# Performance work log

Measured on AMD Instinct MI355X. Metric: run time of the kernel, lower is better.

Reference implementation:

```python
import jax, jax.numpy as jnp
import numpy as np

SAMPLING_RATIO = 1.0


def gcn_conv(x, src, dst, ew, W, b):
    """PyG GCNConv: h = D^-1/2 (A+I) D^-1/2 (xW) + b, edges weighted by ew.
    Masked edges (ew=0) contribute neither messages nor degree, exactly
    matching running the conv on the subset edge_index."""
    n = x.shape[0]
    h = x @ W                                              # [N, out]
    deg = jax.ops.segment_sum(ew, dst, num_segments=n) + 1.0  # +1 for self-loop
    dinv = jax.lax.rsqrt(deg)                              # deg >= 1, safe
    norm = dinv[src] * dinv[dst] * ew                      # [E]
    agg = jax.ops.segment_sum(h[src] * norm[:, None], dst, num_segments=n)
    return agg + h * (dinv * dinv)[:, None] + b            # self-loop term + bias


def setup_inputs() -> dict:
    key = jax.random.key(0)
    ks = jax.random.split(key, 8)
    N, E, F_IN, HID, OUT = 50000, 800000, 128, 128, 64
    x = jax.random.normal(ks[0], (N, F_IN), dtype=jnp.float32)
    edge_index = jax.random.randint(ks[1], (2, E), 0, N, dtype=jnp.int32)
    edge_rand = jax.random.uniform(ks[2], (E,), dtype=jnp.float32)
    s0 = 1.0 / np.sqrt(F_IN)
    s1 = 1.0 / np.sqrt(HID)
    w0 = jax.random.normal(ks[3], (F_IN, HID), dtype=jnp.float32) * s0
    b0 = jnp.zeros((HID,), dtype=jnp.float32)
    w1 = jax.random.normal(ks[4], (HID, HID), dtype=jnp.float32) * s1
    b1 = jnp.zeros((HID,), dtype=jnp.float32)
    w2 = jax.random.normal(ks[5], (HID, OUT), dtype=jnp.float32) * s1
    b2 = jnp.zeros((OUT,), dtype=jnp.float32)
    return {"x": x, "edge_index": edge_index, "edge_rand": edge_rand,
            "w0": w0, "b0": b0, "w1": w1, "b1": b1, "w2": w2, "b2": b2}


def reference(x, edge_index, edge_rand, w0, b0, w1, b1, w2, b2):
    src, dst = edge_index[0], edge_index[1]
    ones = jnp.ones(src.shape, dtype=x.dtype)
    # first pass over full graph -> tmp_z
    z = jax.nn.relu(gcn_conv(x, src, dst, ones, w0, b0))
    z = jax.nn.relu(gcn_conv(z, src, dst, ones, w1, b1))
    tmp_z = gcn_conv(z, src, dst, ones, w2, b2)
    # edge sampling: gather-dot-sigmoid-threshold (detached mask)
    edge_logit = jnp.sum(tmp_z[src] * tmp_z[dst], axis=-1)
    edge_weight = jax.nn.sigmoid(edge_logit)
    mask = jax.lax.stop_gradient(
        (edge_weight > SAMPLING_RATIO * edge_rand).astype(x.dtype))
    # second pass: sampled edges for hidden layers, full edges for last layer
    h = jax.nn.relu(gcn_conv(x, src, dst, mask, w0, b0))
    h = jax.nn.relu(gcn_conv(h, src, dst, mask, w1, b1))
    out = gcn_conv(h, src, dst, ones, w2, b2)
    return out
```

## Files before the change

### kernel.cpp

```cpp
#include <hip/hip_runtime.h>


typedef __attribute__((ext_vector_type(8))) short bf16x8;
typedef __attribute__((ext_vector_type(4))) float f32x4;

__device__ inline unsigned bfpair(float lo, float hi) {
    unsigned a = __float_as_uint(lo), b = __float_as_uint(hi);
    a = (a + 0x7FFFu + ((a >> 16) & 1u)) >> 16;
    b = (b + 0x7FFFu + ((b >> 16) & 1u)) & 0xFFFF0000u;
    return a | b;
}
__device__ inline unsigned short bf1(float v) {
    unsigned u = __float_as_uint(v);
    return (unsigned short)((u + 0x7FFFu + ((u >> 16) & 1u)) >> 16);
}
__device__ inline void unpack2(unsigned u, float& f0, float& f1) {
    f0 = __uint_as_float(u << 16);
    f1 = __uint_as_float(u & 0xFFFF0000u);
}

__global__ void k_scan1(const int* __restrict__ in, int* __restrict__ out,
                        int* __restrict__ bsums, int N) {
    __shared__ int tmp[256];
    int i = blockIdx.x * 256 + threadIdx.x;
    int v = (i < N) ? in[i] : 0;
    tmp[threadIdx.x] = v;
    __syncthreads();
    for (int off = 1; off < 256; off <<= 1) {
        int t = (threadIdx.x >= off) ? tmp[threadIdx.x - off] : 0;
        __syncthreads();
        tmp[threadIdx.x] += t;
        __syncthreads();
    }
    if (i < N) out[i] = tmp[threadIdx.x] - v;
    if (threadIdx.x == 255) bsums[blockIdx.x] = tmp[255];
}

__global__ void k_scan2(int* __restrict__ bsums, int nb) {
    __shared__ int tmp[256];
    int v = (threadIdx.x < nb) ? bsums[threadIdx.x] : 0;
    tmp[threadIdx.x] = v;
    __syncthreads();
    for (int off = 1; off < 256; off <<= 1) {
        int t = (threadIdx.x >= off) ? tmp[threadIdx.x - off] : 0;
        __syncthreads();
        tmp[threadIdx.x] += t;
        __syncthreads();
    }
    if (threadIdx.x < nb) bsums[threadIdx.x] = tmp[threadIdx.x] - v;
}

__global__ void k_scan3(int* __restrict__ out, const int* __restrict__ bsums, int N, int E) {
    int i = blockIdx.x * 256 + threadIdx.x;
    if (i < N) out[i] += bsums[blockIdx.x];
    if (i == 0) out[N] = E;
}

__global__ __launch_bounds__(256) void k_bcount(const int* __restrict__ dst,
                                                int* __restrict__ cnt, int E, int chunk) {
    __shared__ int h[1024];
    for (int i = threadIdx.x; i < 1024; i += 256) h[i] = 0;
    __syncthreads();
    int beg = blockIdx.x * chunk, end = min(E, beg + chunk);
    for (int e = beg + threadIdx.x; e < end; e += 256)
        atomicAdd(&h[dst[e] >> 6], 1);
    __syncthreads();
    for (int b = threadIdx.x; b < 1024; b += 256)
        cnt[b * 64 + blockIdx.x] = h[b];
}

__global__ __launch_bounds__(256) void k_bscatter(const int* __restrict__ src,
                                                  const int* __restrict__ dst,
                                                  const float* __restrict__ er,
                                                  const int* __restrict__ sbase,
                                                  int2* __restrict__ stg, int E, int chunk) {
    __shared__ int cur[1024];
    for (int i = threadIdx.x; i < 1024; i += 256) cur[i] = 0;
    __syncthreads();
    int beg = blockIdx.x * chunk, end = min(E, beg + chunk);
    for (int e = beg + threadIdx.x; e < end; e += 256) {
        int d = dst[e];
        int b = d >> 6;
        int loc = atomicAdd(&cur[b], 1);
        int pos = sbase[b * 64 + blockIdx.x] + loc;
        stg[pos] = make_int2(src[e] | ((d & 63) << 16), (int)__float_as_uint(er[e]));
    }
}

__global__ __launch_bounds__(256) void k_bindeg(const int2* __restrict__ stg,
                                                const int* __restrict__ sbase,
                                                int* __restrict__ indeg,
                                                float* __restrict__ dinvF, int N) {
    __shared__ int cnt[64];
    if (threadIdx.x < 64) cnt[threadIdx.x] = 0;
    __syncthreads();
    int b = blockIdx.x;
    int beg = sbase[b * 64], end = sbase[(b + 1) * 64];
    for (int i = beg + threadIdx.x; i < end; i += 256)
        atomicAdd(&cnt[(stg[i].x >> 16) & 63], 1);
    __syncthreads();
    if (threadIdx.x < 64) {
        int node = b * 64 + threadIdx.x;
        if (node < N) {
            int c = cnt[threadIdx.x];
            indeg[node] = c;
            dinvF[node] = 1.0f / sqrtf((float)c + 1.0f);
        }
    }
}

__global__ __launch_bounds__(256) void k_bfill(const int2* __restrict__ stg,
                                               const int* __restrict__ sbase,
                                               const int* __restrict__ csr_off,
                                               int2* __restrict__ csr_se, int N) {
    __shared__ int cur[64];
    int b = blockIdx.x;
    if (threadIdx.x < 64) {
        int node = b * 64 + threadIdx.x;
        cur[threadIdx.x] = (node < N) ? csr_off[node] : 0;
    }
    __syncthreads();
    int beg = sbase[b * 64], end = sbase[(b + 1) * 64];
    for (int i = beg + threadIdx.x; i < end; i += 256) {
        int2 se = stg[i];
        int j = (se.x >> 16) & 63;
        int pos = atomicAdd(&cur[j], 1);
        csr_se[pos] = make_int2(se.x & 0xFFFF, se.y);
    }
}

__global__ __launch_bounds__(128) void k_surv(const float* __restrict__ tz,
                                              const int* __restrict__ csr_off,
                                              const int2* __restrict__ csr_se,
                                              float* __restrict__ survive,
                                              float* __restrict__ dinvM, int N) {
    const int v = blockIdx.x;
    const int l = threadIdx.x & 15;
    const int s = threadIdx.x >> 4;
    const int e0 = csr_off[v];
    const int e1 = csr_off[v + 1];
    const float4 tv = *(const float4*)&tz[(size_t)v * 64 + l * 4];
    int cnt = 0;
    for (int i = e0 + s; i < e1; i += 8) {
        int2 se = csr_se[i];
        const float4 a = *(const float4*)&tz[(size_t)se.x * 64 + l * 4];
        float p = a.x * tv.x + a.y * tv.y + a.z * tv.z + a.w * tv.w;
        p += __shfl_xor(p, 1, 16);
        p += __shfl_xor(p, 2, 16);
        p += __shfl_xor(p, 4, 16);
        p += __shfl_xor(p, 8, 16);
        float sg = 1.0f / (1.0f + expf(-p));
        float m = (sg > __uint_as_float((unsigned)se.y)) ? 1.0f : 0.0f;
        if (l == 0) {
            survive[i] = m;
            cnt += (m != 0.0f) ? 1 : 0;
        }
    }
    __shared__ int sc[8];
    if (l == 0) sc[s] = cnt;
    __syncthreads();
    if (threadIdx.x == 0) {
        int t = 0;
#pragma unroll
        for (int k = 0; k < 8; k++) t += sc[k];
        dinvM[v] = 1.0f / sqrtf((float)t + 1.0f);
    }
}

__device__ inline void packw3_one(const float* __restrict__ W, unsigned short* __restrict__ Wp,
                                  int OUTC, int idx) {
    int l = idx & 63;
    int tk = idx >> 6;
    int kb = tk & 3;
    int ct = tk >> 2;
    size_t PL = (size_t)(OUTC / 16) * 4 * 64 * 8;
    unsigned short v0[8], v1[8], v2[8];
#pragma unroll
    for (int i = 0; i < 8; i++) {
        float wv = W[(kb * 32 + ((l >> 4) * 8) + i) * OUTC + ct * 16 + (l & 15)];
        unsigned short h0 = bf1(wv);
        float f0 = __uint_as_float((unsigned)h0 << 16);
        float r1 = wv - f0;
        unsigned short h1 = bf1(r1);
        float f1 = __uint_as_float((unsigned)h1 << 16);
        unsigned short h2 = bf1(r1 - f1);
        v0[i] = h0; v1[i] = h1; v2[i] = h2;
    }
    auto st = [](unsigned short* dst, unsigned short* v) {
        uint4 u;
        u.x = v[0] | ((unsigned)v[1] << 16);
        u.y = v[2] | ((unsigned)v[3] << 16);
        u.z = v[4] | ((unsigned)v[5] << 16);
        u.w = v[6] | ((unsigned)v[7] << 16);
        *(uint4*)dst = u;
    };
    st(&Wp[(size_t)idx * 8], v0);
    st(&Wp[PL + (size_t)idx * 8], v1);
    st(&Wp[2 * PL + (size_t)idx * 8], v2);
}

__global__ void k_packw3_all(const float* __restrict__ w0, const float* __restrict__ w1,
                             const float* __restrict__ w2,
                             unsigned short* __restrict__ w0p, unsigned short* __restrict__ w1p,
                             unsigned short* __restrict__ w2p) {
    int b = blockIdx.x;
    if (b < 8) packw3_one(w0, w0p, 128, b * 256 + threadIdx.x);
    else if (b < 16) packw3_one(w1, w1p, 128, (b - 8) * 256 + threadIdx.x);
    else packw3_one(w2, w2p, 64, (b - 16) * 256 + threadIdx.x);
}

template <int OUTC, bool WB16>
__global__ __launch_bounds__(256) void k_gemm_split(const float* __restrict__ A,
                                                    const unsigned short* __restrict__ Wp,
                                                    float* __restrict__ Cout,
                                                    unsigned short* __restrict__ Cb, int N) {
    constexpr int CT = OUTC / 16;
    constexpr int PL = CT * 4 * 64 * 8;
    constexpr int LDW = OUTC + 4;
    __shared__ float eps[64 * LDW];
    const int w = threadIdx.x >> 6;
    const int l = threadIdx.x & 63;
    int row = blockIdx.x * 64 + w * 16 + (l & 15);
    int rowc = (row < N) ? row : (N - 1);

    bf16x8 a0[4], a1[4], a2[4];
#pragma unroll
    for (int kb = 0; kb < 4; kb++) {
        const float* pa = &A[(size_t)rowc * 128 + kb * 32 + ((l >> 4) * 8)];
        float4 x0 = *(const float4*)pa;
        float4 x1 = *(const float4*)(pa + 4);
        float xa[8] = {x0.x, x0.y, x0.z, x0.w, x1.x, x1.y, x1.z, x1.w};
#pragma unroll
        for (int i = 0; i < 8; i++) {
            unsigned short h0 = bf1(xa[i]);
            float f0 = __uint_as_float((unsigned)h0 << 16);
            float r1 = xa[i] - f0;
            unsigned short h1 = bf1(r1);
            float f1 = __uint_as_float((unsigned)h1 << 16);
            unsigned short h2 = bf1(r1 - f1);
            a0[kb][i] = (short)h0;
            a1[kb][i] = (short)h1;
            a2[kb][i] = (short)h2;
        }
    }
#pragma unroll
    for (int ct = 0; ct < CT; ct++) {
        f32x4 accA = {0.f, 0.f, 0.f, 0.f};
        f32x4 accB = {0.f, 0.f, 0.f, 0.f};
#pragma unroll
        for (int kb = 0; kb < 4; kb++) {
            const size_t bo = ((size_t)(ct * 4 + kb) * 64 + l) * 8;
            bf16x8 b0 = *(const bf16x8*)&Wp[bo];
            bf16x8 b1 = *(const bf16x8*)&Wp[PL + bo];
            bf16x8 b2 = *(const bf16x8*)&Wp[2 * PL + bo];
            accA = __builtin_amdgcn_mfma_f32_16x16x32_bf16(a0[kb], b0, accA, 0, 0, 0);
            accB = __builtin_amdgcn_mfma_f32_16x16x32_bf16(a0[kb], b1, accB, 0, 0, 0);
            accA = __builtin_amdgcn_mfma_f32_16x16x32_bf16(a1[kb], b0, accA, 0, 0, 0);
            accB = __builtin_amdgcn_mfma_f32_16x16x32_bf16(a1[kb], b1, accB, 0, 0, 0);
            accA = __builtin_amdgcn_mfma_f32_16x16x32_bf16(a2[kb], b0, accA, 0, 0, 0);
            accB = __builtin_amdgcn_mfma_f32_16x16x32_bf16(a0[kb], b2, accB, 0, 0, 0);
        }
#pragma unroll
        for (int r = 0; r < 4; r++) {
            int rr = w * 16 + (l >> 4) * 4 + r;
            eps[rr * LDW + ct * 16 + (l & 15)] = accA[r] + accB[r];
        }
    }
    __syncthreads();
    constexpr int NF4 = 64 * OUTC / 4;
    for (int idx = threadIdx.x; idx < NF4; idx += 256) {
        int rl = idx / (OUTC / 4);
        int cg = idx % (OUTC / 4);
        int grow = blockIdx.x * 64 + rl;
        if (grow < N) {
            const float* sp = &eps[rl * LDW + cg * 4];
            float4 vv = make_float4(sp[0], sp[1], sp[2], sp[3]);
            *(float4*)&Cout[(size_t)grow * OUTC + cg * 4] = vv;
            if (WB16)
                *(uint2*)&Cb[(size_t)grow * OUTC + cg * 4] =
                    make_uint2(bfpair(vv.x, vv.y), bfpair(vv.z, vv.w));
        }
    }
}

template <int OUTC>
__global__ __launch_bounds__(256) void k_gemm_mfma(const unsigned short* __restrict__ A,
                                                   const unsigned short* __restrict__ Wpk,
                                                   unsigned short* __restrict__ C, int N) {
    constexpr int CT = OUTC / 16;
    __shared__ unsigned short eps[64 * OUTC];
    const int w = threadIdx.x >> 6;
    const int l = threadIdx.x & 63;
    const int rowl = (w * 16) + (l & 15);
    int row = blockIdx.x * 64 + rowl;
    int rowc = (row < N) ? row : (N - 1);

    bf16x8 a[4];
#pragma unroll
    for (int kb = 0; kb < 4; kb++)
        a[kb] = *(const bf16x8*)&A[(size_t)rowc * 128 + kb * 32 + ((l >> 4) * 8)];

#pragma unroll
    for (int ct = 0; ct < CT; ct++) {
        f32x4 acc = {0.f, 0.f, 0.f, 0.f};
#pragma unroll
        for (int kb = 0; kb < 4; kb++) {
            bf16x8 b = *(const bf16x8*)&Wpk[((size_t)(ct * 4 + kb) * 64 + l) * 8];
            acc = __builtin_amdgcn_mfma_f32_16x16x32_bf16(a[kb], b, acc, 0, 0, 0);
        }
#pragma unroll
        for (int r = 0; r < 4; r++) {
            int rr = w * 16 + (l >> 4) * 4 + r;
            eps[rr * OUTC + ct * 16 + (l & 15)] = bf1(acc[r]);
        }
    }
    __syncthreads();
    constexpr int NU4 = 64 * OUTC / 8;
    for (int idx = threadIdx.x; idx < NU4; idx += 256) {
        int rl = idx / (OUTC / 8);
        int cg = idx % (OUTC / 8);
        int grow = blockIdx.x * 64 + rl;
        if (grow < N)
            *(uint4*)&C[(size_t)grow * OUTC + cg * 8] = *(const uint4*)&eps[rl * OUTC + cg * 8];
    }
}

template <bool RELU>
__global__ __launch_bounds__(128) void k_agg128(const float* __restrict__ h,
                                                const int* __restrict__ csr_off,
                                                const int2* __restrict__ csr_se,
                                                const float* __restrict__ dinv,
                                                const float* __restrict__ bias,
                                                float* __restrict__ out, int N) {
    const int v = blockIdx.x;
    const int l = threadIdx.x & 31;
    const int s = threadIdx.x >> 5;
    const int e0 = csr_off[v];
    const int e1 = csr_off[v + 1];
    float4 acc = make_float4(0.f, 0.f, 0.f, 0.f);
    int i = e0 + s;
    for (; i + 4 < e1; i += 8) {
        int sa = csr_se[i].x;      float wa = dinv[sa];
        int sb = csr_se[i + 4].x;  float wb = dinv[sb];
        float4 a = *(const float4*)&h[(size_t)sa * 128 + l * 4];
        float4 b = *(const float4*)&h[(size_t)sb * 128 + l * 4];
        acc.x = fmaf(a.x, wa, acc.x); acc.y = fmaf(a.y, wa, acc.y);
        acc.z = fmaf(a.z, wa, acc.z); acc.w = fmaf(a.w, wa, acc.w);
        acc.x = fmaf(b.x, wb, acc.x); acc.y = fmaf(b.y, wb, acc.y);
        acc.z = fmaf(b.z, wb, acc.z); acc.w = fmaf(b.w, wb, acc.w);
    }
    if (i < e1) {
        int sa = csr_se[i].x;
        float wa = dinv[sa];
        float4 a = *(const float4*)&h[(size_t)sa * 128 + l * 4];
        acc.x = fmaf(a.x, wa, acc.x); acc.y = fmaf(a.y, wa, acc.y);
        acc.z = fmaf(a.z, wa, acc.z); acc.w = fmaf(a.w, wa, acc.w);
    }
    __shared__ float4 red[4][32];
    red[s][l] = acc;
    __syncthreads();
    if (threadIdx.x < 32) {
        float4 r0 = red[0][l], r1 = red[1][l], r2 = red[2][l], r3 = red[3][l];
        float dv = dinv[v];
        float4 hv = *(const float4*)&h[(size_t)v * 128 + l * 4];
        float4 bb = *(const float4*)&bias[l * 4];
        float4 o;
        o.x = dv * ((r0.x + r1.x + r2.x + r3.x) + hv.x * dv) + bb.x;
        o.y = dv * ((r0.y + r1.y + r2.y + r3.y) + hv.y * dv) + bb.y;
        o.z = dv * ((r0.z + r1.z + r2.z + r3.z) + hv.z * dv) + bb.z;
        o.w = dv * ((r0.w + r1.w + r2.w + r3.w) + hv.w * dv) + bb.w;
        if (RELU) {
            o.x = fmaxf(o.x, 0.f); o.y = fmaxf(o.y, 0.f);
            o.z = fmaxf(o.z, 0.f); o.w = fmaxf(o.w, 0.f);
        }
        *(float4*)&out[(size_t)v * 128 + l * 4] = o;
    }
}

__global__ __launch_bounds__(128) void k_agg64(const float* __restrict__ h,
                                               const int* __restrict__ csr_off,
                                               const int2* __restrict__ csr_se,
                                               const float* __restrict__ dinv,
                                               const float* __restrict__ bias,
                                               float* __restrict__ out, int N) {
    const int v = blockIdx.x;
    const int l = threadIdx.x & 15;
    const int s = threadIdx.x >> 4;
    const int e0 = csr_off[v];
    const int e1 = csr_off[v + 1];
    float4 acc = make_float4(0.f, 0.f, 0.f, 0.f);
    int i = e0 + s;
    for (; i + 8 < e1; i += 16) {
        int sa = csr_se[i].x;      float wa = dinv[sa];
        int sb = csr_se[i + 8].x;  float wb = dinv[sb];
        float4 a = *(const float4*)&h[(size_t)sa * 64 + l * 4];
        float4 b = *(const float4*)&h[(size_t)sb * 64 + l * 4];
        acc.x = fmaf(a.x, wa, acc.x); acc.y = fmaf(a.y, wa, acc.y);
        acc.z = fmaf(a.z, wa, acc.z); acc.w = fmaf(a.w, wa, acc.w);
        acc.x = fmaf(b.x, wb, acc.x); acc.y = fmaf(b.y, wb, acc.y);
        acc.z = fmaf(b.z, wb, acc.z); acc.w = fmaf(b.w, wb, acc.w);
    }
    if (i < e1) {
        int sa = csr_se[i].x;
        float wa = dinv[sa];
        float4 a = *(const float4*)&h[(size_t)sa * 64 + l * 4];
        acc.x = fmaf(a.x, wa, acc.x); acc.y = fmaf(a.y, wa, acc.y);
        acc.z = fmaf(a.z, wa, acc.z); acc.w = fmaf(a.w, wa, acc.w);
    }
    __shared__ float4 red[8][16];
    red[s][l] = acc;
    __syncthreads();
    if (threadIdx.x < 16) {
        float4 aa = make_float4(0.f, 0.f, 0.f, 0.f);
#pragma unroll
        for (int k = 0; k < 8; ++k) {
            float4 r = red[k][l];
            aa.x += r.x; aa.y += r.y; aa.z += r.z; aa.w += r.w;
        }
        float dv = dinv[v];
        float4 hv = *(const float4*)&h[(size_t)v * 64 + l * 4];
        float4 bb = *(const float4*)&bias[l * 4];
        float4 o;
        o.x = dv * (aa.x + hv.x * dv) + bb.x;
        o.y = dv * (aa.y + hv.y * dv) + bb.y;
        o.z = dv * (aa.z + hv.z * dv) + bb.z;
        o.w = dv * (aa.w + hv.w * dv) + bb.w;
        *(float4*)&out[(size_t)v * 64 + l * 4] = o;
    }
}

template <bool RELU, bool MASKED>
__global__ __launch_bounds__(128) void k_agg128b(const unsigned short* __restrict__ h,
                                                 const int* __restrict__ csr_off,
                                                 const int2* __restrict__ csr_se,
                                                 const float* __restrict__ survive,
                                                 const float* __restrict__ dinv,
                                                 const float* __restrict__ bias,
                                                 unsigned short* __restrict__ out, int N) {
    const int v = blockIdx.x;
    const int l = threadIdx.x & 15;
    const int s = threadIdx.x >> 4;
    const int e0 = csr_off[v];
    const int e1 = csr_off[v + 1];
    float acc[8];
#pragma unroll
    for (int j = 0; j < 8; j++) acc[j] = 0.f;
    int i = e0 + s;
    for (; i + 8 < e1; i += 16) {
        int sa = csr_se[i].x;
        int sb = csr_se[i + 8].x;
        float wa = MASKED ? dinv[sa] * survive[i] : dinv[sa];
        float wb = MASKED ? dinv[sb] * survive[i + 8] : dinv[sb];
        uint4 ua = *(const uint4*)&h[(size_t)sa * 128 + l * 8];
        uint4 ub = *(const uint4*)&h[(size_t)sb * 128 + l * 8];
        float f0, f1;
        unpack2(ua.x, f0, f1); acc[0] = fmaf(f0, wa, acc[0]); acc[1] = fmaf(f1, wa, acc[1]);
        unpack2(ua.y, f0, f1); acc[2] = fmaf(f0, wa, acc[2]); acc[3] = fmaf(f1, wa, acc[3]);
        unpack2(ua.z, f0, f1); acc[4] = fmaf(f0, wa, acc[4]); acc[5] = fmaf(f1, wa, acc[5]);
        unpack2(ua.w, f0, f1); acc[6] = fmaf(f0, wa, acc[6]); acc[7] = fmaf(f1, wa, acc[7]);
        unpack2(ub.x, f0, f1); acc[0] = fmaf(f0, wb, acc[0]); acc[1] = fmaf(f1, wb, acc[1]);
        unpack2(ub.y, f0, f1); acc[2] = fmaf(f0, wb, acc[2]); acc[3] = fmaf(f1, wb, acc[3]);
        unpack2(ub.z, f0, f1); acc[4] = fmaf(f0, wb, acc[4]); acc[5] = fmaf(f1, wb, acc[5]);
        unpack2(ub.w, f0, f1); acc[6] = fmaf(f0, wb, acc[6]); acc[7] = fmaf(f1, wb, acc[7]);
    }
    if (i < e1) {
        int sa = csr_se[i].x;
        float wa = MASKED ? dinv[sa] * survive[i] : dinv[sa];
        uint4 ua = *(const uint4*)&h[(size_t)sa * 128 + l * 8];
        float f0, f1;
        unpack2(ua.x, f0, f1); acc[0] = fmaf(f0, wa, acc[0]); acc[1] = fmaf(f1, wa, acc[1]);
        unpack2(ua.y, f0, f1); acc[2] = fmaf(f0, wa, acc[2]); acc[3] = fmaf(f1, wa, acc[3]);
        unpack2(ua.z, f0, f1); acc[4] = fmaf(f0, wa, acc[4]); acc[5] = fmaf(f1, wa, acc[5]);
        unpack2(ua.w, f0, f1); acc[6] = fmaf(f0, wa, acc[6]); acc[7] = fmaf(f1, wa, acc[7]);
    }
    __shared__ float red[8][16][8];
#pragma unroll
    for (int j = 0; j < 8; j += 4)
        *(float4*)&red[s][l][j] = make_float4(acc[j], acc[j + 1], acc[j + 2], acc[j + 3]);
    __syncthreads();
    if (threadIdx.x < 16) {
        int ll = threadIdx.x;
        float rr[8];
#pragma unroll
        for (int j = 0; j < 8; j++) rr[j] = 0.f;
#pragma unroll
        for (int k = 0; k < 8; ++k)
#pragma unroll
            for (int j = 0; j < 8; j++) rr[j] += red[k][ll][j];
        float dv = dinv[v];
        uint4 uh = *(const uint4*)&h[(size_t)v * 128 + ll * 8];
        float hv[8];
        unpack2(uh.x, hv[0], hv[1]); unpack2(uh.y, hv[2], hv[3]);
        unpack2(uh.z, hv[4], hv[5]); unpack2(uh.w, hv[6], hv[7]);
        unsigned u[4];
#pragma unroll
        for (int j2 = 0; j2 < 4; j2++) {
            float o0 = dv * (rr[2 * j2 + 0] + hv[2 * j2 + 0] * dv) + bias[ll * 8 + 2 * j2 + 0];
            float o1 = dv * (rr[2 * j2 + 1] + hv[2 * j2 + 1] * dv) + bias[ll * 8 + 2 * j2 + 1];
            if (RELU) { o0 = fmaxf(o0, 0.f); o1 = fmaxf(o1, 0.f); }
            u[j2] = bfpair(o0, o1);
        }
        *(uint4*)&out[(size_t)v * 128 + ll * 8] = make_uint4(u[0], u[1], u[2], u[3]);
    }
}

__global__ __launch_bounds__(128) void k_agg64b(const unsigned short* __restrict__ h,
                                                const int* __restrict__ csr_off,
                                                const int2* __restrict__ csr_se,
                                                const float* __restrict__ dinv,
                                                const float* __restrict__ bias,
                                                float* __restrict__ out, int N) {
    const int v = blockIdx.x;
    const int l = threadIdx.x & 7;
    const int s = threadIdx.x >> 3;
    const int e0 = csr_off[v];
    const int e1 = csr_off[v + 1];
    float acc[8];
#pragma unroll
    for (int j = 0; j < 8; j++) acc[j] = 0.f;
    for (int i = e0 + s; i < e1; i += 16) {
        int sa = csr_se[i].x;
        float wa = dinv[sa];
        uint4 ua = *(const uint4*)&h[(size_t)sa * 64 + l * 8];
        float f0, f1;
        unpack2(ua.x, f0, f1); acc[0] = fmaf(f0, wa, acc[0]); acc[1] = fmaf(f1, wa, acc[1]);
        unpack2(ua.y, f0, f1); acc[2] = fmaf(f0, wa, acc[2]); acc[3] = fmaf(f1, wa, acc[3]);
        unpack2(ua.z, f0, f1); acc[4] = fmaf(f0, wa, acc[4]); acc[5] = fmaf(f1, wa, acc[5]);
        unpack2(ua.w, f0, f1); acc[6] = fmaf(f0, wa, acc[6]); acc[7] = fmaf(f1, wa, acc[7]);
    }
    __shared__ float red[16][8][8];
#pragma unroll
    for (int j = 0; j < 8; j += 4)
        *(float4*)&red[s][l][j] = make_float4(acc[j], acc[j + 1], acc[j + 2], acc[j + 3]);
    __syncthreads();
    if (threadIdx.x < 8) {
        int ll = threadIdx.x;
        float rr[8];
#pragma unroll
        for (int j = 0; j < 8; j++) rr[j] = 0.f;
#pragma unroll
        for (int k = 0; k < 16; ++k)
#pragma unroll
            for (int j = 0; j < 8; j++) rr[j] += red[k][ll][j];
        float dv = dinv[v];
        uint4 uh = *(const uint4*)&h[(size_t)v * 64 + ll * 8];
        float hv[8];
        unpack2(uh.x, hv[0], hv[1]); unpack2(uh.y, hv[2], hv[3]);
        unpack2(uh.z, hv[4], hv[5]); unpack2(uh.w, hv[6], hv[7]);
        float o[8];
#pragma unroll
        for (int j = 0; j < 8; j++) o[j] = dv * (rr[j] + hv[j] * dv) + bias[ll * 8 + j];
        *(float4*)&out[(size_t)v * 64 + ll * 8 + 0] = make_float4(o[0], o[1], o[2], o[3]);
        *(float4*)&out[(size_t)v * 64 + ll * 8 + 4] = make_float4(o[4], o[5], o[6], o[7]);
    }
}

extern "C" void kernel_launch(void* const* d_in, const int* in_sizes, int n_in,
                              void* d_out, int out_size, void* d_ws, size_t ws_size,
                              hipStream_t stream) {
    const float* x  = (const float*)d_in[0];
    const int*   ei = (const int*)d_in[1];
    const float* er = (const float*)d_in[2];
    const float* w0 = (const float*)d_in[3];
    const float* b0 = (const float*)d_in[4];
    const float* w1 = (const float*)d_in[5];
    const float* b1 = (const float*)d_in[6];
    const float* w2 = (const float*)d_in[7];
    const float* b2 = (const float*)d_in[8];
    const int N = in_sizes[0] / 128;
    const int E = in_sizes[2];
    const int* src  = ei;
    const int* dstv = ei + E;
    float* out = (float*)d_out;

    char* p = (char*)d_ws;
    auto alloc = [&](size_t bytes) {
        char* r = p;
        p += (bytes + 255) & ~(size_t)255;
        return r;
    };
    int* indeg     = (int*)alloc((size_t)N * 4);
    int* csr_off   = (int*)alloc((size_t)(N + 1) * 4);
    int* bsums     = (int*)alloc(1024);
    int* bcnt      = (int*)alloc((size_t)65536 * 4);
    int* sbase     = (int*)alloc((size_t)65537 * 4);
    int2* csr_se   = (int2*)alloc((size_t)E * 8);
    int2* stg      = (int2*)alloc((size_t)E * 8);
    float* dinvF   = (float*)alloc((size_t)N * 4);
    float* dinvM   = (float*)alloc((size_t)N * 4);
    float* hx      = (float*)alloc((size_t)N * 128 * 4);
    unsigned short* hxb = (unsigned short*)alloc((size_t)N * 128 * 2);
    float* wk1     = (float*)alloc((size_t)N * 128 * 4);
    float* wk2     = (float*)alloc((size_t)N * 128 * 4);
    float* tz      = (float*)alloc((size_t)N * 64 * 4);
    unsigned short* w0p3 = (unsigned short*)alloc((size_t)3 * 128 * 128 * 2);
    unsigned short* w1p3 = (unsigned short*)alloc((size_t)3 * 128 * 128 * 2);
    unsigned short* w2p3 = (unsigned short*)alloc((size_t)3 * 128 * 64 * 2);
    unsigned short* wk1b = (unsigned short*)wk1;
    unsigned short* wk2b = (unsigned short*)wk2;
    float* survive = (float*)stg;

    const int nb = (N + 255) / 256;
    const int chunk = (E + 63) / 64;

    k_packw3_all<<<20, 256, 0, stream>>>(w0, w1, w2, w0p3, w1p3, w2p3);

    k_bcount<<<64, 256, 0, stream>>>(dstv, bcnt, E, chunk);
    k_scan1<<<256, 256, 0, stream>>>(bcnt, sbase, bsums, 65536);
    k_scan2<<<1, 256, 0, stream>>>(bsums, 256);
    k_scan3<<<256, 256, 0, stream>>>(sbase, bsums, 65536, E);
    k_bscatter<<<64, 256, 0, stream>>>(src, dstv, er, sbase, stg, E, chunk);
    k_bindeg<<<1024, 256, 0, stream>>>(stg, sbase, indeg, dinvF, N);
    k_scan1<<<nb, 256, 0, stream>>>(indeg, csr_off, bsums, N);
    k_scan2<<<1, 256, 0, stream>>>(bsums, nb);
    k_scan3<<<nb, 256, 0, stream>>>(csr_off, bsums, N, E);
    k_bfill<<<1024, 256, 0, stream>>>(stg, sbase, csr_off, csr_se, N);

    const int gbm = (N + 63) / 64;

    k_gemm_split<128, true><<<gbm, 256, 0, stream>>>(x, w0p3, hx, hxb, N);

    k_agg128<true><<<N, 128, 0, stream>>>(hx, csr_off, csr_se, dinvF, b0, wk1, N);
    k_gemm_split<128, false><<<gbm, 256, 0, stream>>>(wk1, w1p3, wk2, nullptr, N);
    k_agg128<true><<<N, 128, 0, stream>>>(wk2, csr_off, csr_se, dinvF, b1, wk1, N);
    k_gemm_split<64, false><<<gbm, 256, 0, stream>>>(wk1, w2p3, wk2, nullptr, N);
    k_agg64<<<N, 128, 0, stream>>>(wk2, csr_off, csr_se, dinvF, b2, tz, N);

    k_surv<<<N, 128, 0, stream>>>(tz, csr_off, csr_se, survive, dinvM, N);

    k_agg128b<true, true><<<N, 128, 0, stream>>>(hxb, csr_off, csr_se, survive, dinvM, b0, wk1b, N);
    k_gemm_mfma<128><<<gbm, 256, 0, stream>>>(wk1b, w1p3, wk2b, N);
    k_agg128b<true, true><<<N, 128, 0, stream>>>(wk2b, csr_off, csr_se, survive, dinvM, b1, wk1b, N);
    k_gemm_mfma<64><<<gbm, 256, 0, stream>>>(wk1b, w2p3, wk2b, N);
    k_agg64b<<<N, 128, 0, stream>>>(wk2b, csr_off, csr_se, dinvF, b2, out, N);
}
```

Measured before the change: 492.0 us.

## Map one wavefront per node in aggregation kernels, reduce with shuffles

All six aggregation kernels now give each node a single 64-lane wavefront, with four nodes per 256-thread block, instead of one 128-thread block per node. The cross-slice reduction uses __shfl_xor instead of shared memory and __syncthreads. This is meant to cut block-scheduling overhead and idle threads on low-degree nodes (about 16 edges each) and to remove the LDS round-trip and barrier. In exchange, fewer edges are in flight per node, so each wave has less memory-level parallelism for the gathers.

```diff
diff --git a/kernel.cpp b/kernel.cpp
--- a/kernel.cpp
+++ b/kernel.cpp
@@ -326,15 +326,70 @@
 }
 
 template <bool RELU>
-__global__ __launch_bounds__(128) void k_agg128(const float* __restrict__ h,
+__global__ __launch_bounds__(256) void k_agg128(const float* __restrict__ h,
                                                 const int* __restrict__ csr_off,
                                                 const int2* __restrict__ csr_se,
                                                 const float* __restrict__ dinv,
                                                 const float* __restrict__ bias,
                                                 float* __restrict__ out, int N) {
-    const int v = blockIdx.x;
-    const int l = threadIdx.x & 31;
-    const int s = threadIdx.x >> 5;
+    const int v = blockIdx.x * 4 + (threadIdx.x >> 6);
+    if (v >= N) return;
+    const int lane = threadIdx.x & 63;
+    const int l = lane & 31;
+    const int s = lane >> 5;
+    const int e0 = csr_off[v];
+    const int e1 = csr_off[v + 1];
+    float4 acc = make_float4(0.f, 0.f, 0.f, 0.f);
+    int i = e0 + s;
+    for (; i + 2 < e1; i += 4) {
+        int sa = csr_se[i].x;      float wa = dinv[sa];
+        int sb = csr_se[i + 2].x;  float wb = dinv[sb];
+        float4 a = *(const float4*)&h[(size_t)sa * 128 + l * 4];
+        float4 b = *(const float4*)&h[(size_t)sb * 128 + l * 4];
+        acc.x = fmaf(a.x, wa, acc.x); acc.y = fmaf(a.y, wa, acc.y);
+        acc.z = fmaf(a.z, wa, acc.z); acc.w = fmaf(a.w, wa, acc.w);
+        acc.x = fmaf(b.x, wb, acc.x); acc.y = fmaf(b.y, wb, acc.y);
+        acc.z = fmaf(b.z, wb, acc.z); acc.w = fmaf(b.w, wb, acc.w);
+    }
+    if (i < e1) {
+        int sa = csr_se[i].x;
+        float wa = dinv[sa];
+        float4 a = *(const float4*)&h[(size_t)sa * 128 + l * 4];
+        acc.x = fmaf(a.x, wa, acc.x); acc.y = fmaf(a.y, wa, acc.y);
+        acc.z = fmaf(a.z, wa, acc.z); acc.w = fmaf(a.w, wa, acc.w);
+    }
+    acc.x += __shfl_xor(acc.x, 32);
+    acc.y += __shfl_xor(acc.y, 32);
+    acc.z += __shfl_xor(acc.z, 32);
+    acc.w += __shfl_xor(acc.w, 32);
+    if (s == 0) {
+        float dv = dinv[v];
+        float4 hv = *(const float4*)&h[(size_t)v * 128 + l * 4];
+        float4 bb = *(const float4*)&bias[l * 4];
+        float4 o;
+        o.x = dv * (acc.x + hv.x * dv) + bb.x;
+        o.y = dv * (acc.y + hv.y * dv) + bb.y;
+        o.z = dv * (acc.z + hv.z * dv) + bb.z;
+        o.w = dv * (acc.w + hv.w * dv) + bb.w;
+        if (RELU) {
+            o.x = fmaxf(o.x, 0.f); o.y = fmaxf(o.y, 0.f);
+            o.z = fmaxf(o.z, 0.f); o.w = fmaxf(o.w, 0.f);
+        }
+        *(float4*)&out[(size_t)v * 128 + l * 4] = o;
+    }
+}
+
+__global__ __launch_bounds__(256) void k_agg64(const float* __restrict__ h,
+                                               const int* __restrict__ csr_off,
+                                               const int2* __restrict__ csr_se,
+                                               const float* __restrict__ dinv,
+                                               const float* __restrict__ bias,
+                                               float* __restrict__ out, int N) {
+    const int v = blockIdx.x * 4 + (threadIdx.x >> 6);
+    if (v >= N) return;
+    const int lane = threadIdx.x & 63;
+    const int l = lane & 15;
+    const int s = lane >> 4;
     const int e0 = csr_off[v];
     const int e1 = csr_off[v + 1];
     float4 acc = make_float4(0.f, 0.f, 0.f, 0.f);
@@ -342,57 +397,6 @@
     for (; i + 4 < e1; i += 8) {
         int sa = csr_se[i].x;      float wa = dinv[sa];
         int sb = csr_se[i + 4].x;  float wb = dinv[sb];
-        float4 a = *(const float4*)&h[(size_t)sa * 128 + l * 4];
-        float4 b = *(const float4*)&h[(size_t)sb * 128 + l * 4];
-        acc.x = fmaf(a.x, wa, acc.x); acc.y = fmaf(a.y, wa, acc.y);
-        acc.z = fmaf(a.z, wa, acc.z); acc.w = fmaf(a.w, wa, acc.w);
-        acc.x = fmaf(b.x, wb, acc.x); acc.y = fmaf(b.y, wb, acc.y);
-        acc.z = fmaf(b.z, wb, acc.z); acc.w = fmaf(b.w, wb, acc.w);
-    }
-    if (i < e1) {
-        int sa = csr_se[i].x;
-        float wa = dinv[sa];
-        float4 a = *(const float4*)&h[(size_t)sa * 128 + l * 4];
-        acc.x = fmaf(a.x, wa, acc.x); acc.y = fmaf(a.y, wa, acc.y);
-        acc.z = fmaf(a.z, wa, acc.z); acc.w = fmaf(a.w, wa, acc.w);
-    }
-    __shared__ float4 red[4][32];
-    red[s][l] = acc;
-    __syncthreads();
-    if (threadIdx.x < 32) {
-        float4 r0 = red[0][l], r1 = red[1][l], r2 = red[2][l], r3 = red[3][l];
-        float dv = dinv[v];
-        float4 hv = *(const float4*)&h[(size_t)v * 128 + l * 4];
-        float4 bb = *(const float4*)&bias[l * 4];
-        float4 o;
-        o.x = dv * ((r0.x + r1.x + r2.x + r3.x) + hv.x * dv) + bb.x;
-        o.y = dv * ((r0.y + r1.y + r2.y + r3.y) + hv.y * dv) + bb.y;
-        o.z = dv * ((r0.z + r1.z + r2.z + r3.z) + hv.z * dv) + bb.z;
-        o.w = dv * ((r0.w + r1.w + r2.w + r3.w) + hv.w * dv) + bb.w;
-        if (RELU) {
-            o.x = fmaxf(o.x, 0.f); o.y = fmaxf(o.y, 0.f);
-            o.z = fmaxf(o.z, 0.f); o.w = fmaxf(o.w, 0.f);
-        }
-        *(float4*)&out[(size_t)v * 128 + l * 4] = o;
-    }
-}
-
-__global__ __launch_bounds__(128) void k_agg64(const float* __restrict__ h,
-                                               const int* __restrict__ csr_off,
-                                               const int2* __restrict__ csr_se,
-                                               const float* __restrict__ dinv,
-                                               const float* __restrict__ bias,
-                                               float* __restrict__ out, int N) {
-    const int v = blockIdx.x;
-    const int l = threadIdx.x & 15;
-    const int s = threadIdx.x >> 4;
-    const int e0 = csr_off[v];
-    const int e1 = csr_off[v + 1];
-    float4 acc = make_float4(0.f, 0.f, 0.f, 0.f);
-    int i = e0 + s;
-    for (; i + 8 < e1; i += 16) {
-        int sa = csr_se[i].x;      float wa = dinv[sa];
-        int sb = csr_se[i + 8].x;  float wb = dinv[sb];
         float4 a = *(const float4*)&h[(size_t)sa * 64 + l * 4];
         float4 b = *(const float4*)&h[(size_t)sb * 64 + l * 4];
         acc.x = fmaf(a.x, wa, acc.x); acc.y = fmaf(a.y, wa, acc.y);
@@ -407,50 +411,47 @@
         acc.x = fmaf(a.x, wa, acc.x); acc.y = fmaf(a.y, wa, acc.y);
         acc.z = fmaf(a.z, wa, acc.z); acc.w = fmaf(a.w, wa, acc.w);
     }
-    __shared__ float4 red[8][16];
-    red[s][l] = acc;
-    __syncthreads();
-    if (threadIdx.x < 16) {
-        float4 aa = make_float4(0.f, 0.f, 0.f, 0.f);
-#pragma unroll
-        for (int k = 0; k < 8; ++k) {
-            float4 r = red[k][l];
-            aa.x += r.x; aa.y += r.y; aa.z += r.z; aa.w += r.w;
-        }
+    acc.x += __shfl_xor(acc.x, 32); acc.y += __shfl_xor(acc.y, 32);
+    acc.z += __shfl_xor(acc.z, 32); acc.w += __shfl_xor(acc.w, 32);
+    acc.x += __shfl_xor(acc.x, 16); acc.y += __shfl_xor(acc.y, 16);
+    acc.z += __shfl_xor(acc.z, 16); acc.w += __shfl_xor(acc.w, 16);
+    if (s == 0) {
         float dv = dinv[v];
         float4 hv = *(const float4*)&h[(size_t)v * 64 + l * 4];
         float4 bb = *(const float4*)&bias[l * 4];
         float4 o;
-        o.x = dv * (aa.x + hv.x * dv) + bb.x;
-        o.y = dv * (aa.y + hv.y * dv) + bb.y;
-        o.z = dv * (aa.z + hv.z * dv) + bb.z;
-        o.w = dv * (aa.w + hv.w * dv) + bb.w;
+        o.x = dv * (acc.x + hv.x * dv) + bb.x;
+        o.y = dv * (acc.y + hv.y * dv) + bb.y;
+        o.z = dv * (acc.z + hv.z * dv) + bb.z;
+        o.w = dv * (acc.w + hv.w * dv) + bb.w;
         *(float4*)&out[(size_t)v * 64 + l * 4] = o;
     }
 }
 
-template <bool RELU, bool MASKED>
-__global__ __launch_bounds__(128) void k_agg128b(const unsigned short* __restrict__ h,
+template <bool RELU>
+__global__ __launch_bounds__(256) void k_agg128b(const unsigned short* __restrict__ h,
                                                  const int* __restrict__ csr_off,
                                                  const int2* __restrict__ csr_se,
                                                  const float* __restrict__ survive,
                                                  const float* __restrict__ dinv,
                                                  const float* __restrict__ bias,
                                                  unsigned short* __restrict__ out, int N) {
-    const int v = blockIdx.x;
-    const int l = threadIdx.x & 15;
-    const int s = threadIdx.x >> 4;
+    const int v = blockIdx.x * 4 + (threadIdx.x >> 6);
+    if (v >= N) return;
+    const int lane = threadIdx.x & 63;
+    const int l = lane & 15;
+    const int s = lane >> 4;
     const int e0 = csr_off[v];
     const int e1 = csr_off[v + 1];
     float acc[8];
 #pragma unroll
     for (int j = 0; j < 8; j++) acc[j] = 0.f;
     int i = e0 + s;
-    for (; i + 8 < e1; i += 16) {
+    for (; i + 4 < e1; i += 8) {
         int sa = csr_se[i].x;
-        int sb = csr_se[i + 8].x;
-        float wa = MASKED ? dinv[sa] * survive[i] : dinv[sa];
-        float wb = MASKED ? dinv[sb] * survive[i + 8] : dinv[sb];
+        int sb = csr_se[i + 4].x;
+        float wa = dinv[sa] * survive[i];
+        float wb = dinv[sb] * survive[i + 4];
         uint4 ua = *(const uint4*)&h[(size_t)sa * 128 + l * 8];
         uint4 ub = *(const uint4*)&h[(size_t)sb * 128 + l * 8];
         float f0, f1;
@@ -465,7 +466,7 @@
     }
     if (i < e1) {
         int sa = csr_se[i].x;
-        float wa = MASKED ? dinv[sa] * survive[i] : dinv[sa];
+        float wa = dinv[sa] * survive[i];
         uint4 ua = *(const uint4*)&h[(size_t)sa * 128 + l * 8];
         float f0, f1;
         unpack2(ua.x, f0, f1); acc[0] = fmaf(f0, wa, acc[0]); acc[1] = fmaf(f1, wa, acc[1]);
@@ -473,52 +474,45 @@
         unpack2(ua.z, f0, f1); acc[4] = fmaf(f0, wa, acc[4]); acc[5] = fmaf(f1, wa, acc[5]);
         unpack2(ua.w, f0, f1); acc[6] = fmaf(f0, wa, acc[6]); acc[7] = fmaf(f1, wa, acc[7]);
     }
-    __shared__ float red[8][16][8];
-#pragma unroll
-    for (int j = 0; j < 8; j += 4)
-        *(float4*)&red[s][l][j] = make_float4(acc[j], acc[j + 1], acc[j + 2], acc[j + 3]);
-    __syncthreads();
-    if (threadIdx.x < 16) {
-        int ll = threadIdx.x;
-        float rr[8];
-#pragma unroll
-        for (int j = 0; j < 8; j++) rr[j] = 0.f;
-#pragma unroll
-        for (int k = 0; k < 8; ++k)
-#pragma unroll
-            for (int j = 0; j < 8; j++) rr[j] += red[k][ll][j];
+#pragma unroll
+    for (int j = 0; j < 8; j++) acc[j] += __shfl_xor(acc[j], 32);
+#pragma unroll
+    for (int j = 0; j < 8; j++) acc[j] += __shfl_xor(acc[j], 16);
+    if (s == 0) {
         float dv = dinv[v];
-        uint4 uh = *(const uint4*)&h[(size_t)v * 128 + ll * 8];
+        uint4 uh = *(const uint4*)&h[(size_t)v * 128 + l * 8];
         float hv[8];
         unpack2(uh.x, hv[0], hv[1]); unpack2(uh.y, hv[2], hv[3]);
         unpack2(uh.z, hv[4], hv[5]); unpack2(uh.w, hv[6], hv[7]);
         unsigned u[4];
 #pragma unroll
         for (int j2 = 0; j2 < 4; j2++) {
-            float o0 = dv * (rr[2 * j2 + 0] + hv[2 * j2 + 0] * dv) + bias[ll * 8 + 2 * j2 + 0];
-            float o1 = dv * (rr[2 * j2 + 1] + hv[2 * j2 + 1] * dv) + bias[ll * 8 + 2 * j2 + 1];
+            float o0 = dv * (acc[2 * j2 + 0] + hv[2 * j2 + 0] * dv) + bias[l * 8 + 2 * j2 + 0];
+            float o1 = dv * (acc[2 * j2 + 1] + hv[2 * j2 + 1] * dv) + bias[l * 8 + 2 * j2 + 1];
             if (RELU) { o0 = fmaxf(o0, 0.f); o1 = fmaxf(o1, 0.f); }
             u[j2] = bfpair(o0, o1);
         }
-        *(uint4*)&out[(size_t)v * 128 + ll * 8] = make_uint4(u[0], u[1], u[2], u[3]);
-    }
-}
-
-__global__ __launch_bounds__(128) void k_agg64b(const unsigned short* __restrict__ h,
+        *(uint4*)&out[(size_t)v * 128 + l * 8] = make_uint4(u[0], u[1], u[2], u[3]);
+    }
+}
+
+__global__ __launch_bounds__(256) void k_agg64b(const unsigned short* __restrict__ h,
                                                 const int* __restrict__ csr_off,
                                                 const int2* __restrict__ csr_se,
                                                 const float* __restrict__ dinv,
                                                 const float* __restrict__ bias,
                                                 float* __restrict__ out, int N) {
-    const int v = blockIdx.x;
-    const int l = threadIdx.x & 7;
-    const int s = threadIdx.x >> 3;
+    const int v = blockIdx.x * 4 + (threadIdx.x >> 6);
+    if (v >= N) return;
+    const int lane = threadIdx.x & 63;
+    const int l = lane & 7;
+    const int s = lane >> 3;
     const int e0 = csr_off[v];
     const int e1 = csr_off[v + 1];
     float acc[8];
 #pragma unroll
     for (int j = 0; j < 8; j++) acc[j] = 0.f;
-    for (int i = e0 + s; i < e1; i += 16) {
+    for (int i = e0 + s; i < e1; i += 8) {
         int sa = csr_se[i].x;
         float wa = dinv[sa];
         uint4 ua = *(const uint4*)&h[(size_t)sa * 64 + l * 8];
@@ -528,30 +522,23 @@
         unpack2(ua.z, f0, f1); acc[4] = fmaf(f0, wa, acc[4]); acc[5] = fmaf(f1, wa, acc[5]);
         unpack2(ua.w, f0, f1); acc[6] = fmaf(f0, wa, acc[6]); acc[7] = fmaf(f1, wa, acc[7]);
     }
-    __shared__ float red[16][8][8];
-#pragma unroll
-    for (int j = 0; j < 8; j += 4)
-        *(float4*)&red[s][l][j] = make_float4(acc[j], acc[j + 1], acc[j + 2], acc[j + 3]);
-    __syncthreads();
-    if (threadIdx.x < 8) {
-        int ll = threadIdx.x;
-        float rr[8];
-#pragma unroll
-        for (int j = 0; j < 8; j++) rr[j] = 0.f;
-#pragma unroll
-        for (int k = 0; k < 16; ++k)
-#pragma unroll
-            for (int j = 0; j < 8; j++) rr[j] += red[k][ll][j];
+#pragma unroll
+    for (int j = 0; j < 8; j++) acc[j] += __shfl_xor(acc[j], 32);
+#pragma unroll
+    for (int j = 0; j < 8; j++) acc[j] += __shfl_xor(acc[j], 16);
+#pragma unroll
+    for (int j = 0; j < 8; j++) acc[j] += __shfl_xor(acc[j], 8);
+    if (s == 0) {
         float dv = dinv[v];
-        uint4 uh = *(const uint4*)&h[(size_t)v * 64 + ll * 8];
+        uint4 uh = *(const uint4*)&h[(size_t)v * 64 + l * 8];
         float hv[8];
         unpack2(uh.x, hv[0], hv[1]); unpack2(uh.y, hv[2], hv[3]);
         unpack2(uh.z, hv[4], hv[5]); unpack2(uh.w, hv[6], hv[7]);
         float o[8];
 #pragma unroll
-        for (int j = 0; j < 8; j++) o[j] = dv * (rr[j] + hv[j] * dv) + bias[ll * 8 + j];
-        *(float4*)&out[(size_t)v * 64 + ll * 8 + 0] = make_float4(o[0], o[1], o[2], o[3]);
-        *(float4*)&out[(size_t)v * 64 + ll * 8 + 4] = make_float4(o[4], o[5], o[6], o[7]);
+        for (int j = 0; j < 8; j++) o[j] = dv * (acc[j] + hv[j] * dv) + bias[l * 8 + j];
+        *(float4*)&out[(size_t)v * 64 + l * 8 + 0] = make_float4(o[0], o[1], o[2], o[3]);
+        *(float4*)&out[(size_t)v * 64 + l * 8 + 4] = make_float4(o[4], o[5], o[6], o[7]);
     }
 }
 
@@ -617,20 +604,21 @@
     k_bfill<<<1024, 256, 0, stream>>>(stg, sbase, csr_off, csr_se, N);
 
     const int gbm = (N + 63) / 64;
+    const int ga = (N + 3) / 4;
 
     k_gemm_split<128, true><<<gbm, 256, 0, stream>>>(x, w0p3, hx, hxb, N);
 
-    k_agg128<true><<<N, 128, 0, stream>>>(hx, csr_off, csr_se, dinvF, b0, wk1, N);
+    k_agg128<true><<<ga, 256, 0, stream>>>(hx, csr_off, csr_se, dinvF, b0, wk1, N);
     k_gemm_split<128, false><<<gbm, 256, 0, stream>>>(wk1, w1p3, wk2, nullptr, N);
-    k_agg128<true><<<N, 128, 0, stream>>>(wk2, csr_off, csr_se, dinvF, b1, wk1, N);
+    k_agg128<true><<<ga, 256, 0, stream>>>(wk2, csr_off, csr_se, dinvF, b1, wk1, N);
     k_gemm_split<64, false><<<gbm, 256, 0, stream>>>(wk1, w2p3, wk2, nullptr, N);
-    k_agg64<<<N, 128, 0, stream>>>(wk2, csr_off, csr_se, dinvF, b2, tz, N);
+    k_agg64<<<ga, 256, 0, stream>>>(wk2, csr_off, csr_se, dinvF, b2, tz, N);
 
     k_surv<<<N, 128, 0, stream>>>(tz, csr_off, csr_se, survive, dinvM, N);
 
-    k_agg128b<true, true><<<N, 128, 0, stream>>>(hxb, csr_off, csr_se, survive, dinvM, b0, wk1b, N);
+    k_agg128b<true><<<ga, 256, 0, stream>>>(hxb, csr_off, csr_se, survive, dinvM, b0, wk1b, N);
     k_gemm_mfma<128><<<gbm, 256, 0, stream>>>(wk1b, w1p3, wk2b, N);
-    k_agg128b<true, true><<<N, 128, 0, stream>>>(wk2b, csr_off, csr_se, survive, dinvM, b1, wk1b, N);
+    k_agg128b<true><<<ga, 256, 0, stream>>>(wk2b, csr_off, csr_se, survive, dinvM, b1, wk1b, N);
     k_gemm_mfma<64><<<gbm, 256, 0, stream>>>(wk1b, w2p3, wk2b, N);
-    k_agg64b<<<N, 128, 0, stream>>>(wk2b, csr_off, csr_se, dinvF, b2, out, N);
-}
+    k_agg64b<<<ga, 256, 0, stream>>>(wk2b, csr_off, csr_se, dinvF, b2, out, N);
+}
```

Measured after the change: 462.5 us. 6.0% less time.
